# Optimization experiments

Hardware: AMD Instinct MI355X
Metric: run time of the kernel (lower is better)

Reference implementation:

```python
import jax, jax.numpy as jnp
import numpy as np

IN_CH = 256
LATENT = 32

def setup_inputs() -> dict:
    key = jax.random.key(0)
    k1, k2, k3 = jax.random.split(key, 3)
    x = jax.random.normal(k1, (8, IN_CH, 64, 64), dtype=jnp.float32)
    # 1x1 conv weights stored as [out, in] matrices
    w_qk = jax.random.normal(k2, (2 * LATENT, IN_CH), dtype=jnp.float32) * (IN_CH ** -0.5)
    w_v = jax.random.normal(k3, (IN_CH, IN_CH), dtype=jnp.float32) * (IN_CH ** -0.5)
    gamma = jnp.zeros((1,), dtype=jnp.float32) + 0.5  # nonzero so attention path matters
    return {"x": x, "w_qk": w_qk, "w_v": w_v, "gamma": gamma}

def reference(x, w_qk, w_v, gamma):
    b, c, h, w = x.shape
    xf = x.reshape(b, c, h * w)                      # [b, c, s]
    qk = jnp.einsum('oc,bcs->bos', w_qk, xf)          # 1x1 conv == matmul
    q, k = qk[:, :LATENT], qk[:, LATENT:]             # [b, L, s] each
    v = jnp.einsum('oc,bcs->bos', w_v, xf)            # [b, c, s]
    scale = 1.0 / LATENT ** 0.25
    m = jnp.einsum('bcs,bct->bst', scale * q, scale * k)  # [b, s, s]
    m = jax.nn.softmax(m, axis=-1)
    a = jnp.einsum('bst,bct->bcs', m, v)              # [b, c, s]
    a = a.reshape(b, c, h, w)
    return gamma * a + x
```

## Files before the change

### kernel.cpp

```cpp
#include <hip/hip_runtime.h>

typedef __attribute__((ext_vector_type(4)))  float f32x4;
typedef __attribute__((ext_vector_type(16))) float f32x16;
typedef __attribute__((ext_vector_type(8)))  short short8;
typedef __attribute__((ext_vector_type(4)))  unsigned short u16x4;
typedef __attribute__((ext_vector_type(4)))  unsigned int u32x4;
typedef __attribute__((ext_vector_type(2)))  unsigned int u32x2;

static __device__ __forceinline__ unsigned short f2bf(float f) {
    unsigned int u = __float_as_uint(f);
    unsigned int r = (u + 0x7FFFu + ((u >> 16) & 1u)) >> 16;
    return (unsigned short)r;
}

#if __has_builtin(__builtin_amdgcn_exp2f)
#define EXP2(x) __builtin_amdgcn_exp2f(x)
#else
#define EXP2(x) exp2f(x)
#endif

static __device__ __forceinline__ u32x2 swap32v(unsigned int a, unsigned int b) {
#if __has_builtin(__builtin_amdgcn_permlane32_swap)
    return __builtin_amdgcn_permlane32_swap(a, b, false, false);
#else
    asm("v_permlane32_swap_b32 %0, %1" : "+v"(a), "+v"(b));
    u32x2 r; r[0] = a; r[1] = b; return r;
#endif
}

static __device__ __forceinline__ void block_sync_lds() {
    asm volatile("s_waitcnt lgkmcnt(0)" ::: "memory");
    __builtin_amdgcn_s_barrier();
    asm volatile("" ::: "memory");
}

#define SCALE2Q 0.25503487756f

__global__ void prep_w_kernel(const float* __restrict__ wqk,
                              const float* __restrict__ wv,
                              unsigned short* __restrict__ W) {
    int idx = blockIdx.x * 256 + threadIdx.x;
    int o = idx >> 8, c = idx & 255;
    float v;
    if (o < 64) { v = wqk[o * 256 + c]; if (o < 32) v *= SCALE2Q; }
    else        { v = wv[(o - 64) * 256 + c]; }
    W[idx] = f2bf(v);
}

__global__ __launch_bounds__(256) void transpose_kernel(
        const float* __restrict__ x, unsigned short* __restrict__ xT) {
    __shared__ unsigned short tile[64][66];
    int b = blockIdx.x & 7;
    int rem = blockIdx.x >> 3;
    int ct = rem >> 6, st = rem & 63;
    int s0 = st * 64, c0 = ct * 64;
    int tid = threadIdx.x;
    int ss = tid & 63, cq = tid >> 6;
#pragma unroll
    for (int p = 0; p < 16; ++p) {
        int cc = p * 4 + cq;
        float v = x[(size_t)(b * 256 + c0 + cc) * 4096 + s0 + ss];
        tile[ss][cc] = f2bf(v);
    }
    __syncthreads();
#pragma unroll
    for (int p = 0; p < 8; ++p) {
        int idx = p * 256 + tid;
        int sr = idx >> 5, jj = idx & 31;
        unsigned int val = *(const unsigned int*)&tile[sr][jj * 2];
        *(unsigned int*)(xT + (size_t)(b * 4096 + s0 + sr) * 256 + c0 + jj * 2) = val;
    }
}

__global__ __launch_bounds__(256) void proj_kernel(
        const unsigned short* __restrict__ W,
        const unsigned short* __restrict__ xT,
        unsigned short* __restrict__ qkT,
        unsigned short* __restrict__ vbuf) {
    const int b  = blockIdx.x & 7;
    const int sb = blockIdx.x >> 3;
    const int s0 = sb * 64;
    const int tid = threadIdx.x;
    const int w = tid >> 6, l = tid & 63;
    const int lg = l >> 4, ll = l & 15;
    const size_t xbase = (size_t)b * 4096 * 256;

    f32x4 acc[5][4];
#pragma unroll
    for (int ot = 0; ot < 5; ++ot)
#pragma unroll
        for (int st = 0; st < 4; ++st) acc[ot][st] = (f32x4)0.0f;

    for (int k0 = 0; k0 < 256; k0 += 32) {
        short8 bf[4], af[5];
#pragma unroll
        for (int st = 0; st < 4; ++st)
            bf[st] = *(const short8*)(xT + xbase + (size_t)(s0 + st * 16 + ll) * 256 + k0 + lg * 8);
#pragma unroll
        for (int ot = 0; ot < 5; ++ot)
            af[ot] = *(const short8*)(W + (size_t)(80 * w + ot * 16 + ll) * 256 + k0 + lg * 8);
#pragma unroll
        for (int ot = 0; ot < 5; ++ot)
#pragma unroll
            for (int st = 0; st < 4; ++st)
                acc[ot][st] = __builtin_amdgcn_mfma_f32_16x16x32_bf16(af[ot], bf[st], acc[ot][st], 0, 0, 0);
    }
#pragma unroll
    for (int ot = 0; ot < 5; ++ot) {
        int o0 = 80 * w + ot * 16 + lg * 4;
#pragma unroll
        for (int st = 0; st < 4; ++st) {
            int s = s0 + st * 16 + ll;
            if (o0 < 64) {
                u16x4 pk;
#pragma unroll
                for (int i = 0; i < 4; ++i) pk[i] = f2bf(acc[ot][st][i]);
                *(u16x4*)(qkT + (size_t)b * 4096 * 64 + (size_t)s * 64 + o0) = pk;
            } else {
#pragma unroll
                for (int i = 0; i < 4; ++i)
                    vbuf[(size_t)b * 256 * 4096 + (size_t)(o0 - 64 + i) * 4096 + s] = f2bf(acc[ot][st][i]);
            }
        }
    }
}

__global__ __launch_bounds__(256) void repack_v_kernel(
        const unsigned short* __restrict__ vbuf,
        unsigned short* __restrict__ vfrag) {
    int idx = blockIdx.x * 256 + threadIdx.x;
    int l    = idx & 63;
    int kf16 = (idx >> 6) & 255;
    int ct4  = (idx >> 14) & 7;
    int b    = idx >> 17;
    int l31 = l & 31, l5 = l >> 5;
    short8 v = *(const short8*)(vbuf + (size_t)b * 256 * 4096
                                + (size_t)(32 * ct4 + l31) * 4096
                                + 16 * kf16 + 8 * l5);
    *(short8*)(vfrag + (size_t)idx * 8) = v;
}

__global__ __launch_bounds__(256) void repack_k_kernel(
        const unsigned short* __restrict__ qkT,
        unsigned short* __restrict__ kfrag) {
    int idx = blockIdx.x * 256 + threadIdx.x;
    int l  = idx & 63;
    int h  = (idx >> 6) & 1;
    int t2 = (idx >> 7) & 127;
    int b  = idx >> 14;
    int l31 = l & 31, l5 = l >> 5;
    short8 v = *(const short8*)(qkT + (size_t)b * 4096 * 64
                                + (size_t)(32 * t2 + l31) * 64
                                + 32 + 16 * h + 8 * l5);
    *(short8*)(kfrag + (size_t)idx * 8) = v;
}

__global__ __launch_bounds__(768, 3) void attn_kernel(
        const unsigned short* __restrict__ qkT,
        const unsigned short* __restrict__ kfrag,
        const unsigned short* __restrict__ vfrag,
        const float* __restrict__ x,
        const float* __restrict__ gamma,
        float* __restrict__ out) {
    __shared__ unsigned short p_lds[2][4][4][64][8];
    __shared__ float lsum_lds[128];

    const int b   = blockIdx.x & 7;
    const int sb  = blockIdx.x >> 3;
    const int s0  = sb * 128;
    const int w   = threadIdx.x >> 6;
    const int l   = threadIdx.x & 63;
    const int l5  = l >> 5, l31 = l & 31;

    const size_t qk_base = (size_t)b * 4096 * 64;
    const size_t bx_base = (size_t)b * 256 * 4096;

    if (w < 4) {
        const unsigned short* qrow = qkT + qk_base + (size_t)(s0 + 32 * w + l31) * 64;
        const short8 qf0 = *(const short8*)(qrow + 8 * l5);
        const short8 qf1 = *(const short8*)(qrow + 16 + 8 * l5);
        const unsigned short* kfp = kfrag + (size_t)b * 128 * 2 * 512 + 8 * l;
        const f32x16 z16 = (f32x16)0.0f;
        float psum = 0.f;

        short8 kf00 = *(const short8*)(kfp + 0 * 512);
        short8 kf01 = *(const short8*)(kfp + 1 * 512);
        short8 kf10 = *(const short8*)(kfp + 2 * 512);
        short8 kf11 = *(const short8*)(kfp + 3 * 512);

#define EXPPACK(DD, PLO, PHI)                                                  \
    {                                                                          \
        float e0 = EXP2((DD)[0]),   e1 = EXP2((DD)[1]);                        \
        float e2 = EXP2((DD)[2]),   e3 = EXP2((DD)[3]);                        \
        float e4 = EXP2((DD)[4]),   e5 = EXP2((DD)[5]);                        \
        float e6 = EXP2((DD)[6]),   e7 = EXP2((DD)[7]);                        \
        float e8 = EXP2((DD)[8]),   e9 = EXP2((DD)[9]);                        \
        float e10 = EXP2((DD)[10]), e11 = EXP2((DD)[11]);                      \
        float e12 = EXP2((DD)[12]), e13 = EXP2((DD)[13]);                      \
        float e14 = EXP2((DD)[14]), e15 = EXP2((DD)[15]);                      \
        psum += (((e0 + e1) + (e2 + e3)) + ((e4 + e5) + (e6 + e7)))            \
              + (((e8 + e9) + (e10 + e11)) + ((e12 + e13) + (e14 + e15)));     \
        unsigned int c0, c1, c2, c3;                                           \
        asm("v_cvt_pk_bf16_f32 %0, %1, %2" : "=v"(c0) : "v"(e0), "v"(e1));     \
        asm("v_cvt_pk_bf16_f32 %0, %1, %2" : "=v"(c1) : "v"(e2), "v"(e3));     \
        asm("v_cvt_pk_bf16_f32 %0, %1, %2" : "=v"(c2) : "v"(e4), "v"(e5));     \
        asm("v_cvt_pk_bf16_f32 %0, %1, %2" : "=v"(c3) : "v"(e6), "v"(e7));     \
        u32x2 s0_ = swap32v(c0, c2);                                           \
        u32x2 s1_ = swap32v(c1, c3);                                           \
        u32x4 lo_; lo_[0] = s0_[0]; lo_[1] = s1_[0]; lo_[2] = s0_[1]; lo_[3] = s1_[1]; \
        PLO = __builtin_bit_cast(short8, lo_);                                 \
        unsigned int d0, d1, d2, d3;                                           \
        asm("v_cvt_pk_bf16_f32 %0, %1, %2" : "=v"(d0) : "v"(e8), "v"(e9));     \
        asm("v_cvt_pk_bf16_f32 %0, %1, %2" : "=v"(d1) : "v"(e10), "v"(e11));   \
        asm("v_cvt_pk_bf16_f32 %0, %1, %2" : "=v"(d2) : "v"(e12), "v"(e13));   \
        u32x2 s2_ = swap32v(d0, d2);                                           \
        asm("v_cvt_pk_bf16_f32 %0, %1, %2" : "=v"(d3) : "v"(e14), "v"(e15));   \
        u32x2 s3_ = swap32v(d1, d3);                                           \
        u32x4 hi_; hi_[0] = s2_[0]; hi_[1] = s3_[0]; hi_[2] = s2_[1]; hi_[3] = s3_[1]; \
        PHI = __builtin_bit_cast(short8, hi_);                                 \
    }

#define PRODUCE(T)                                                             \
    {                                                                          \
        const int tn_ = ((T) + 1) & 63;                                        \
        const int pb_ = (T) & 1;                                               \
        f32x16 dd0 = __builtin_amdgcn_mfma_f32_32x32x16_bf16(kf00, qf0, z16, 0, 0, 0); \
        dd0 = __builtin_amdgcn_mfma_f32_32x32x16_bf16(kf01, qf1, dd0, 0, 0, 0);\
        f32x16 dd1 = __builtin_amdgcn_mfma_f32_32x32x16_bf16(kf10, qf0, z16, 0, 0, 0); \
        dd1 = __builtin_amdgcn_mfma_f32_32x32x16_bf16(kf11, qf1, dd1, 0, 0, 0);\
        kf00 = *(const short8*)(kfp + (size_t)(4 * tn_ + 0) * 512);            \
        kf01 = *(const short8*)(kfp + (size_t)(4 * tn_ + 1) * 512);            \
        kf10 = *(const short8*)(kfp + (size_t)(4 * tn_ + 2) * 512);            \
        kf11 = *(const short8*)(kfp + (size_t)(4 * tn_ + 3) * 512);            \
        short8 pa0, pa1, pa2, pa3;                                             \
        EXPPACK(dd0, pa0, pa1)                                                 \
        EXPPACK(dd1, pa2, pa3)                                                 \
        *(short8*)&p_lds[pb_][w][0][l][0] = pa0;                               \
        *(short8*)&p_lds[pb_][w][1][l][0] = pa1;                               \
        *(short8*)&p_lds[pb_][w][2][l][0] = pa2;                               \
        *(short8*)&p_lds[pb_][w][3][l][0] = pa3;                               \
    }

        PRODUCE(0)
        for (int t = 1; t < 64; ++t) {
            block_sync_lds();
            PRODUCE(t)
        }
        block_sync_lds();
#undef PRODUCE
#undef EXPPACK

        psum += __shfl_xor(psum, 32);
        if (l5 == 0) lsum_lds[32 * w + l31] = psum;
        __syncthreads();
    } else {
        const int cw = w - 4;
        const int ch = 32 * cw + l31;
        const unsigned short* vfp = vfrag + ((size_t)(b * 8 + cw) * 256) * 512 + 8 * l;

        f32x16 acc0 = (f32x16)0.0f, acc1 = (f32x16)0.0f;
        f32x16 acc2 = (f32x16)0.0f, acc3 = (f32x16)0.0f;
        short8 vf0 = *(const short8*)(vfp + 0 * 512);
        short8 vf1 = *(const short8*)(vfp + 1 * 512);
        short8 vf2 = *(const short8*)(vfp + 2 * 512);
        short8 vf3 = *(const short8*)(vfp + 3 * 512);

#define CKS(KS, VF)                                                            \
        {                                                                      \
            short8 p0 = *(const short8*)&p_lds[pb][0][KS][l][0];               \
            short8 p1 = *(const short8*)&p_lds[pb][1][KS][l][0];               \
            short8 p2 = *(const short8*)&p_lds[pb][2][KS][l][0];               \
            short8 p3 = *(const short8*)&p_lds[pb][3][KS][l][0];               \
            acc0 = __builtin_amdgcn_mfma_f32_32x32x16_bf16(p0, VF, acc0, 0, 0, 0); \
            acc1 = __builtin_amdgcn_mfma_f32_32x32x16_bf16(p1, VF, acc1, 0, 0, 0); \
            acc2 = __builtin_amdgcn_mfma_f32_32x32x16_bf16(p2, VF, acc2, 0, 0, 0); \
            acc3 = __builtin_amdgcn_mfma_f32_32x32x16_bf16(p3, VF, acc3, 0, 0, 0); \
            VF = *(const short8*)(vfp + (size_t)(4 * tn + (KS)) * 512);        \
        }

        for (int t = 0; t < 64; ++t) {
            block_sync_lds();
            const int pb = t & 1;
            const int tn = (t + 1) & 63;
            CKS(0, vf0)
            CKS(1, vf1)
            CKS(2, vf2)
            CKS(3, vf3)
        }
#undef CKS
        __syncthreads();

        const float g = gamma[0];
#pragma unroll
        for (int rq = 0; rq < 4; ++rq) {
            const int rbase = 8 * rq + 4 * l5;
#define STORE_QB(ACC, QB)                                                      \
            {                                                                  \
                f32x4 ls = *(const f32x4*)&lsum_lds[32 * (QB) + rbase];        \
                f32x4 gi;                                                      \
                gi[0] = g / ls[0]; gi[1] = g / ls[1];                          \
                gi[2] = g / ls[2]; gi[3] = g / ls[3];                          \
                size_t off = bx_base + (size_t)ch * 4096 + s0 + 32 * (QB) + rbase; \
                f32x4 xv = *(const f32x4*)(x + off);                           \
                f32x4 o;                                                       \
                o[0] = gi[0] * (ACC)[4 * rq + 0] + xv[0];                      \
                o[1] = gi[1] * (ACC)[4 * rq + 1] + xv[1];                      \
                o[2] = gi[2] * (ACC)[4 * rq + 2] + xv[2];                      \
                o[3] = gi[3] * (ACC)[4 * rq + 3] + xv[3];                      \
                *(f32x4*)(out + off) = o;                                      \
            }
            STORE_QB(acc0, 0)
            STORE_QB(acc1, 1)
            STORE_QB(acc2, 2)
            STORE_QB(acc3, 3)
#undef STORE_QB
        }
    }
}

extern "C" void kernel_launch(void* const* d_in, const int* in_sizes, int n_in,
                              void* d_out, int out_size, void* d_ws, size_t ws_size,
                              hipStream_t stream) {
    const float* x     = (const float*)d_in[0];
    const float* wqk   = (const float*)d_in[1];
    const float* wv    = (const float*)d_in[2];
    const float* gamma = (const float*)d_in[3];
    float* out = (float*)d_out;

    char* ws = (char*)d_ws;
    unsigned short* W     = (unsigned short*)(ws);
    unsigned short* qkT   = (unsigned short*)(ws + 163840);
    unsigned short* xT    = (unsigned short*)(ws + 4358144);
    unsigned short* vbuf  = (unsigned short*)(ws + 21135360);
    unsigned short* kfrag = (unsigned short*)(ws + 37912576);
    unsigned short* vfrag = xT;

    hipLaunchKernelGGL(prep_w_kernel,    dim3(320),  dim3(256), 0, stream, wqk, wv, W);
    hipLaunchKernelGGL(transpose_kernel, dim3(2048), dim3(256), 0, stream, x, xT);
    hipLaunchKernelGGL(proj_kernel,      dim3(512),  dim3(256), 0, stream, W, xT, qkT, vbuf);
    hipLaunchKernelGGL(repack_v_kernel,  dim3(4096), dim3(256), 0, stream, vbuf, vfrag);
    hipLaunchKernelGGL(repack_k_kernel,  dim3(512),  dim3(256), 0, stream, qkT, kfrag);
    hipLaunchKernelGGL(attn_kernel,      dim3(256),  dim3(768), 0, stream, qkT, kfrag, vfrag, x, gamma, out);
}
```

Measured before the change: 146.1 us.

## Halve consumer waves by giving each PV wave two channel tiles

Shrinks the attention block from 12 to 8 waves so that each consumer wave computes two 32-channel tiles against the same P fragments from LDS. Each LDS read of P now feeds twice as many MFMAs, and the block has fewer waves contending at barriers. The cost is doubled accumulator registers per consumer wave (128 fp32 accumulators) and fewer waves available to hide latency, with occupancy bounds dropping to 512 threads and 2 blocks.

New measurement: 143.8 us. Within noise of the previous version (-1.5%).

```diff
diff --git a/kernel.cpp b/kernel.cpp
--- a/kernel.cpp
+++ b/kernel.cpp
@@ -155,7 +155,7 @@
     *(short8*)(kfrag + (size_t)idx * 8) = v;
 }
 
-__global__ __launch_bounds__(768, 3) void attn_kernel(
+__global__ __launch_bounds__(512, 2) void attn_kernel(
         const unsigned short* __restrict__ qkT,
         const unsigned short* __restrict__ kfrag,
         const unsigned short* __restrict__ vfrag,
@@ -255,37 +255,51 @@
         __syncthreads();
     } else {
         const int cw = w - 4;
-        const int ch = 32 * cw + l31;
-        const unsigned short* vfp = vfrag + ((size_t)(b * 8 + cw) * 256) * 512 + 8 * l;
-
-        f32x16 acc0 = (f32x16)0.0f, acc1 = (f32x16)0.0f;
-        f32x16 acc2 = (f32x16)0.0f, acc3 = (f32x16)0.0f;
-        short8 vf0 = *(const short8*)(vfp + 0 * 512);
-        short8 vf1 = *(const short8*)(vfp + 1 * 512);
-        short8 vf2 = *(const short8*)(vfp + 2 * 512);
-        short8 vf3 = *(const short8*)(vfp + 3 * 512);
-
-#define CKS(KS, VF)                                                            \
+        const int ct0 = 2 * cw, ct1 = 2 * cw + 1;
+        const unsigned short* vfp0 = vfrag + ((size_t)(b * 8 + ct0) * 256) * 512 + 8 * l;
+        const unsigned short* vfp1 = vfrag + ((size_t)(b * 8 + ct1) * 256) * 512 + 8 * l;
+
+        f32x16 a00 = (f32x16)0.0f, a10 = (f32x16)0.0f;
+        f32x16 a20 = (f32x16)0.0f, a30 = (f32x16)0.0f;
+        f32x16 a01 = (f32x16)0.0f, a11 = (f32x16)0.0f;
+        f32x16 a21 = (f32x16)0.0f, a31 = (f32x16)0.0f;
+        short8 vA0 = *(const short8*)(vfp0 + 0 * 512);
+        short8 vA1 = *(const short8*)(vfp1 + 0 * 512);
+        short8 vB0 = *(const short8*)(vfp0 + 1 * 512);
+        short8 vB1 = *(const short8*)(vfp1 + 1 * 512);
+
+#define CKS(KS, V0, V1)                                                        \
         {                                                                      \
             short8 p0 = *(const short8*)&p_lds[pb][0][KS][l][0];               \
             short8 p1 = *(const short8*)&p_lds[pb][1][KS][l][0];               \
             short8 p2 = *(const short8*)&p_lds[pb][2][KS][l][0];               \
             short8 p3 = *(const short8*)&p_lds[pb][3][KS][l][0];               \
-            acc0 = __builtin_amdgcn_mfma_f32_32x32x16_bf16(p0, VF, acc0, 0, 0, 0); \
-            acc1 = __builtin_amdgcn_mfma_f32_32x32x16_bf16(p1, VF, acc1, 0, 0, 0); \
-            acc2 = __builtin_amdgcn_mfma_f32_32x32x16_bf16(p2, VF, acc2, 0, 0, 0); \
-            acc3 = __builtin_amdgcn_mfma_f32_32x32x16_bf16(p3, VF, acc3, 0, 0, 0); \
-            VF = *(const short8*)(vfp + (size_t)(4 * tn + (KS)) * 512);        \
+            a00 = __builtin_amdgcn_mfma_f32_32x32x16_bf16(p0, V0, a00, 0, 0, 0); \
+            a10 = __builtin_amdgcn_mfma_f32_32x32x16_bf16(p1, V0, a10, 0, 0, 0); \
+            a20 = __builtin_amdgcn_mfma_f32_32x32x16_bf16(p2, V0, a20, 0, 0, 0); \
+            a30 = __builtin_amdgcn_mfma_f32_32x32x16_bf16(p3, V0, a30, 0, 0, 0); \
+            a01 = __builtin_amdgcn_mfma_f32_32x32x16_bf16(p0, V1, a01, 0, 0, 0); \
+            a11 = __builtin_amdgcn_mfma_f32_32x32x16_bf16(p1, V1, a11, 0, 0, 0); \
+            a21 = __builtin_amdgcn_mfma_f32_32x32x16_bf16(p2, V1, a21, 0, 0, 0); \
+            a31 = __builtin_amdgcn_mfma_f32_32x32x16_bf16(p3, V1, a31, 0, 0, 0); \
         }
 
         for (int t = 0; t < 64; ++t) {
             block_sync_lds();
             const int pb = t & 1;
             const int tn = (t + 1) & 63;
-            CKS(0, vf0)
-            CKS(1, vf1)
-            CKS(2, vf2)
-            CKS(3, vf3)
+            CKS(0, vA0, vA1)
+            vA0 = *(const short8*)(vfp0 + (size_t)(4 * t + 2) * 512);
+            vA1 = *(const short8*)(vfp1 + (size_t)(4 * t + 2) * 512);
+            CKS(1, vB0, vB1)
+            vB0 = *(const short8*)(vfp0 + (size_t)(4 * t + 3) * 512);
+            vB1 = *(const short8*)(vfp1 + (size_t)(4 * t + 3) * 512);
+            CKS(2, vA0, vA1)
+            vA0 = *(const short8*)(vfp0 + (size_t)(4 * tn + 0) * 512);
+            vA1 = *(const short8*)(vfp1 + (size_t)(4 * tn + 0) * 512);
+            CKS(3, vB0, vB1)
+            vB0 = *(const short8*)(vfp0 + (size_t)(4 * tn + 1) * 512);
+            vB1 = *(const short8*)(vfp1 + (size_t)(4 * tn + 1) * 512);
         }
 #undef CKS
         __syncthreads();
@@ -294,13 +308,13 @@
 #pragma unroll
         for (int rq = 0; rq < 4; ++rq) {
             const int rbase = 8 * rq + 4 * l5;
-#define STORE_QB(ACC, QB)                                                      \
+#define STORE_QB(ACC, QB, CT)                                                  \
             {                                                                  \
                 f32x4 ls = *(const f32x4*)&lsum_lds[32 * (QB) + rbase];        \
                 f32x4 gi;                                                      \
                 gi[0] = g / ls[0]; gi[1] = g / ls[1];                          \
                 gi[2] = g / ls[2]; gi[3] = g / ls[3];                          \
-                size_t off = bx_base + (size_t)ch * 4096 + s0 + 32 * (QB) + rbase; \
+                size_t off = bx_base + (size_t)(32 * (CT) + l31) * 4096 + s0 + 32 * (QB) + rbase; \
                 f32x4 xv = *(const f32x4*)(x + off);                           \
                 f32x4 o;                                                       \
                 o[0] = gi[0] * (ACC)[4 * rq + 0] + xv[0];                      \
@@ -309,10 +323,14 @@
                 o[3] = gi[3] * (ACC)[4 * rq + 3] + xv[3];                      \
                 *(f32x4*)(out + off) = o;                                      \
             }
-            STORE_QB(acc0, 0)
-            STORE_QB(acc1, 1)
-            STORE_QB(acc2, 2)
-            STORE_QB(acc3, 3)
+            STORE_QB(a00, 0, ct0)
+            STORE_QB(a10, 1, ct0)
+            STORE_QB(a20, 2, ct0)
+            STORE_QB(a30, 3, ct0)
+            STORE_QB(a01, 0, ct1)
+            STORE_QB(a11, 1, ct1)
+            STORE_QB(a21, 2, ct1)
+            STORE_QB(a31, 3, ct1)
 #undef STORE_QB
         }
     }
@@ -340,5 +358,5 @@
     hipLaunchKernelGGL(proj_kernel,      dim3(512),  dim3(256), 0, stream, W, xT, qkT, vbuf);
     hipLaunchKernelGGL(repack_v_kernel,  dim3(4096), dim3(256), 0, stream, vbuf, vfrag);
     hipLaunchKernelGGL(repack_k_kernel,  dim3(512),  dim3(256), 0, stream, qkT, kfrag);
-    hipLaunchKernelGGL(attn_kernel,      dim3(256),  dim3(768), 0, stream, qkT, kfrag, vfrag, x, gamma, out);
-}
+    hipLaunchKernelGGL(attn_kernel,      dim3(256),  dim3(512), 0, stream, qkT, kfrag, vfrag, x, gamma, out);
+}
```
